# Performance work log

Hardware: AMD Instinct MI355X
Metric: run time of the kernel (lower is better)

## Reference

```python
import jax, jax.numpy as jnp
import numpy as np

GROUPS = 8
EPS = 1e-5


def setup_inputs() -> dict:
    key = jax.random.key(0)
    ks = jax.random.split(key, 7)
    B, C, H, W = 16, 512, 32, 32
    x = jax.random.normal(ks[0], (B, C, H, W), dtype=jnp.float32)
    norm_w = jnp.ones((C,), jnp.float32)
    norm_b = jnp.zeros((C,), jnp.float32)
    qkv_w = jax.random.normal(ks[1], (3 * C, C), dtype=jnp.float32) * (1.0 / np.sqrt(C))
    qkv_b = jnp.zeros((3 * C,), jnp.float32)
    proj_w = jax.random.normal(ks[2], (C, C), dtype=jnp.float32) * (1.0 / np.sqrt(C))
    proj_b = jnp.zeros((C,), jnp.float32)
    num_heads = 8
    return {"x": x, "norm_w": norm_w, "norm_b": norm_b, "qkv_w": qkv_w,
            "qkv_b": qkv_b, "proj_w": proj_w, "proj_b": proj_b,
            "num_heads": num_heads}


def reference(x, norm_w, norm_b, qkv_w, qkv_b, proj_w, proj_b, num_heads):
    b, c, h, w = x.shape
    n = h * w
    x_in = x
    # GroupNorm(8, c): normalize over (channels-in-group, spatial)
    xg = x.reshape(b, GROUPS, c // GROUPS, n)
    mean = jnp.mean(xg, axis=(2, 3), keepdims=True)
    var = jnp.var(xg, axis=(2, 3), keepdims=True)
    xn = (xg - mean) * jax.lax.rsqrt(var + EPS)
    xn = xn.reshape(b, c, n) * norm_w[None, :, None] + norm_b[None, :, None]
    # 1x1 Conv1d == per-position matmul
    qkv = jnp.einsum('oc,bcn->bon', qkv_w, xn) + qkv_b[None, :, None]
    q, k, v = jnp.split(qkv, 3, axis=1)
    d = c // num_heads
    q = q.reshape(b, num_heads, d, n)
    k = k.reshape(b, num_heads, d, n)
    v = v.reshape(b, num_heads, d, n)
    scale = 1.0 / np.sqrt(d).astype(np.float32)
    # note: scale applied to BOTH q and k (as in the torch source)
    attn = jnp.einsum('bhdn,bhdm->bhnm', q * scale, k * scale)
    attn = jax.nn.softmax(attn, axis=-1)
    out = jnp.einsum('bhnm,bhdm->bhdn', attn, v).reshape(b, c, n)
    out = jnp.einsum('oc,bcn->bon', proj_w, out) + proj_b[None, :, None]
    return out.reshape(b, c, h, w) + x_in
```

## Files before the change

### kernel.cpp

```cpp
#include <hip/hip_runtime.h>

#define NB 16
#define NC 512
#define NSP 1024
#define OQKV 1536
#define EPSV 1e-5f

typedef unsigned short u16;
typedef unsigned int u32;
typedef __attribute__((ext_vector_type(8))) short short8;
typedef __attribute__((ext_vector_type(4))) float f32x4;

__device__ __forceinline__ float us2f(u16 u) {
  return __uint_as_float(((u32)u) << 16);
}
__device__ __forceinline__ u16 f2us(float f) {
  u32 x = __float_as_uint(f);
  return (u16)((x + 0x7fffu + ((x >> 16) & 1u)) >> 16);
}
#if __has_builtin(__builtin_amdgcn_cvt_pk_bf16_f32)
typedef __attribute__((ext_vector_type(2))) __bf16 bf16x2_t;
__device__ __forceinline__ u32 pack2(float a, float b) {
  bf16x2_t r = __builtin_amdgcn_cvt_pk_bf16_f32(a, b);
  return *reinterpret_cast<u32*>(&r);
}
#else
__device__ __forceinline__ u32 pack2(float a, float b) {
  return (u32)f2us(a) | ((u32)f2us(b) << 16);
}
#endif
__device__ __forceinline__ float ld1(const void* p, size_t i, bool f32) {
  return f32 ? ((const float*)p)[i] : us2f(((const u16*)p)[i]);
}
__device__ __forceinline__ bool detect_f32(const void* x0) {
  const u32* xw = (const u32*)x0;
  u32 w = xw[threadIdx.x & 63];
  u32 e = ((w & 0xffffu) >> 7) & 0xffu;
  bool sane = (e >= 0x60u && e <= 0x9fu);
  return __popcll(__ballot(sane)) < 32;
}

typedef const __attribute__((address_space(1))) unsigned int* gas_t;
typedef __attribute__((address_space(3))) unsigned int* las_t;
__device__ __forceinline__ void gload16(const void* g, void* l) {
  __builtin_amdgcn_global_load_lds((gas_t)g, (las_t)l, 16, 0, 0);
}

__global__ __launch_bounds__(256) void gn_partial(
    const void* __restrict__ x, float2* __restrict__ part) {
  bool f32 = detect_f32(x);
  int idx = blockIdx.x;
  size_t base = (size_t)idx * 32768;
  float s1 = 0.f, s2 = 0.f;
  for (int i = threadIdx.x; i < 4096; i += 256) {
    float f[8];
    if (f32) {
      float4 a = *((const float4*)x + (base >> 2) + i * 2);
      float4 b = *((const float4*)x + (base >> 2) + i * 2 + 1);
      f[0]=a.x; f[1]=a.y; f[2]=a.z; f[3]=a.w; f[4]=b.x; f[5]=b.y; f[6]=b.z; f[7]=b.w;
    } else {
      uint4 p = *((const uint4*)x + (base >> 3) + i);
      f[0]=us2f((u16)(p.x&0xffffu)); f[1]=us2f((u16)(p.x>>16));
      f[2]=us2f((u16)(p.y&0xffffu)); f[3]=us2f((u16)(p.y>>16));
      f[4]=us2f((u16)(p.z&0xffffu)); f[5]=us2f((u16)(p.z>>16));
      f[6]=us2f((u16)(p.w&0xffffu)); f[7]=us2f((u16)(p.w>>16));
    }
#pragma unroll
    for (int m = 0; m < 8; m++) { s1 += f[m]; s2 += f[m] * f[m]; }
  }
  __shared__ float r1[256], r2[256];
  r1[threadIdx.x] = s1; r2[threadIdx.x] = s2;
  __syncthreads();
  for (int s = 128; s > 0; s >>= 1) {
    if ((int)threadIdx.x < s) {
      r1[threadIdx.x] += r1[threadIdx.x + s];
      r2[threadIdx.x] += r2[threadIdx.x + s];
    }
    __syncthreads();
  }
  if (threadIdx.x == 0) part[idx] = make_float2(r1[0], r2[0]);
}

__global__ __launch_bounds__(256) void prep_all(
    const void* __restrict__ x, const float2* __restrict__ part,
    const void* __restrict__ gamma, const void* __restrict__ beta,
    const void* __restrict__ qkvw, const void* __restrict__ projw,
    u16* __restrict__ wq, u16* __restrict__ wp, u16* __restrict__ xnt) {
  bool f32 = detect_f32(x);
  int p = blockIdx.x;
  int t = threadIdx.x;
  if (p < 512) {
    const void* src = (p < 384) ? qkvw : projw;
    u16* dst = (p < 384) ? wq : wp;
    size_t e = ((size_t)(p < 384 ? p : p - 384) * 256 + t) * 8;
    uint4 v;
    if (f32) {
      float4 a = *(const float4*)((const float*)src + e);
      float4 b = *(const float4*)((const float*)src + e + 4);
      v.x = pack2(a.x, a.y); v.y = pack2(a.z, a.w);
      v.z = pack2(b.x, b.y); v.w = pack2(b.z, b.w);
    } else {
      v = *(const uint4*)((const u16*)src + e);
    }
    *(uint4*)(dst + e) = v;
    return;
  }
  int q = p - 512;
  int b = q >> 7;
  int c0 = ((q >> 4) & 7) << 6;
  int n0 = (q & 15) << 6;
  __shared__ __align__(16) u16 T[64 * 64];
  int cc = t >> 4;
  int nn = (t & 15) << 2;
  float2 pa = part[((b << 3) + (c0 >> 6)) * 2];
  float2 pb = part[((b << 3) + (c0 >> 6)) * 2 + 1];
  float mean = (pa.x + pb.x) * (1.f / 65536.f);
  float var = (pa.y + pb.y) * (1.f / 65536.f) - mean * mean;
  float inv = rsqrtf(var + EPSV);
#pragma unroll
  for (int rep = 0; rep < 4; rep++) {
    int cl = cc + (rep << 4);
    int c = c0 + cl;
    float g = ld1(gamma, c, f32), be = ld1(beta, c, f32);
    float wsc = g * inv, bsc = be - mean * wsc;
    size_t xb = ((size_t)b * NC + c) * NSP + n0 + nn;
    float f[4];
    if (f32) {
      float4 v = *(const float4*)((const float*)x + xb);
      f[0]=v.x; f[1]=v.y; f[2]=v.z; f[3]=v.w;
    } else {
      uint2 v = *(const uint2*)((const u16*)x + xb);
      f[0]=us2f((u16)(v.x&0xffffu)); f[1]=us2f((u16)(v.x>>16));
      f[2]=us2f((u16)(v.y&0xffffu)); f[3]=us2f((u16)(v.y>>16));
    }
#pragma unroll
    for (int j = 0; j < 4; j++) {
      int n = nn + j;
      T[(n << 6) + (((cl & ~7) ^ ((n & 7) << 3)) | (cl & 7))] =
          f2us(fmaf(f[j], wsc, bsc));
    }
  }
  __syncthreads();
#pragma unroll
  for (int i = 0; i < 2; i++) {
    int slot = (i << 8) + t;
    int nl = slot >> 3;
    int cs = (slot & 7) << 3;
    uint4 v = *(const uint4*)&T[(nl << 6) + (cs ^ ((nl & 7) << 3))];
    *(uint4*)&xnt[((size_t)b * NSP + n0 + nl) * NC + c0 + cs] = v;
  }
}

template <bool OUTRAW, bool RES>
__global__ __launch_bounds__(256) void mfma_gemm(
    const u16* __restrict__ W, const u16* __restrict__ Xt,
    const void* __restrict__ xdet, const void* __restrict__ bias,
    const void* __restrict__ res, void* __restrict__ out, int O) {
  bool f32 = detect_f32(xdet);
  bool of = OUTRAW && f32;
  int gy = O >> 7;
  int bpb = gy << 3;
  int p = blockIdx.x + (blockIdx.y << 3) + blockIdx.z * bpb;
  int k = p >> 3;
  int b = ((p & 7) << 1) + (k >= bpb ? 1 : 0);
  int r = k - (k >= bpb ? bpb : 0);
  int orow = (r >> 3) << 7;
  int ncol = (r & 7) << 7;
  int t = threadIdx.x;
  int lane = t & 63, w = t >> 6;
  int wo = (w >> 1) << 6, wn = (w & 1) << 6;
  int l15 = lane & 15, quad = lane >> 4;

  __shared__ __align__(16) u16 Alds[128 * 64];
  __shared__ __align__(16) u16 Blds[128 * 64];

  f32x4 acc[4][4];
#pragma unroll
  for (int i = 0; i < 4; i++)
#pragma unroll
    for (int j = 0; j < 4; j++) acc[i][j] = (f32x4){0.f, 0.f, 0.f, 0.f};

  int srow = t >> 3;
  int seg = (t & 7) ^ (srow & 7);
  const u16* wpA = W + (size_t)(orow + srow) * NC + (seg << 3);
  const u16* xpB = Xt + ((size_t)b * NSP + ncol + srow) * NC + (seg << 3);

  for (int k0 = 0; k0 < NC; k0 += 64) {
    __syncthreads();
#pragma unroll
    for (int i = 0; i < 4; i++) {
      gload16(wpA + k0 + (size_t)i * (32 * NC), &Alds[(i << 11) + (w << 9)]);
      gload16(xpB + k0 + (size_t)i * (32 * NC), &Blds[(i << 11) + (w << 9)]);
    }
    __syncthreads();
#pragma unroll
    for (int kk = 0; kk < 2; kk++) {
      short8 af[4], bf[4];
#pragma unroll
      for (int ot = 0; ot < 4; ot++) {
        int rr = wo + ot * 16 + l15;
        af[ot] = *(const short8*)&Alds[(rr << 6) + ((((kk << 2) + quad) ^ (rr & 7)) << 3)];
      }
#pragma unroll
      for (int nt = 0; nt < 4; nt++) {
        int rr = wn + nt * 16 + l15;
        bf[nt] = *(const short8*)&Blds[(rr << 6) + ((((kk << 2) + quad) ^ (rr & 7)) << 3)];
      }
#pragma unroll
      for (int ot = 0; ot < 4; ot++)
#pragma unroll
        for (int nt = 0; nt < 4; nt++)
          acc[ot][nt] = __builtin_amdgcn_mfma_f32_16x16x32_bf16(
              af[ot], bf[nt], acc[ot][nt], 0, 0, 0);
    }
  }
#pragma unroll
  for (int ot = 0; ot < 4; ot++) {
#pragma unroll
    for (int rr = 0; rr < 4; rr++) {
      int o = orow + wo + ot * 16 + (quad << 2) + rr;
      float bs = ld1(bias, o, f32);
      size_t rowb = ((size_t)b * O + o) * NSP + ncol + wn + l15;
#pragma unroll
      for (int nt = 0; nt < 4; nt++) {
        size_t idx = rowb + nt * 16;
        float v = acc[ot][nt][rr] + bs;
        if (RES) v += ld1(res, idx, f32);
        if (of) ((float*)out)[idx] = v;
        else ((u16*)out)[idx] = f2us(v);
      }
    }
  }
}

__global__ __launch_bounds__(512, 4) void attn_kernel(
    const u16* __restrict__ qkv, u16* __restrict__ OT) {
  int d = blockIdx.x;
  int blk = ((((d & 7) << 4) | (d >> 5)) << 2) | ((d >> 3) & 3);
  int b = blk >> 5;
  int h = (blk >> 2) & 7;
  int q0 = (blk & 3) << 8;
  int t = threadIdx.x;
  int lane = t & 63, w = t >> 6;
  int l15 = lane & 15, quad = lane >> 4;

  __shared__ __align__(16) u16 Klds[64 * 72];
  __shared__ __align__(16) u16 Vlds[64 * 72];
  __shared__ __align__(16) u16 Plds[8][32 * 72];

  size_t hb = (size_t)b * OQKV + h * 64;

  short8 qf[2][2];
#pragma unroll
  for (int qt = 0; qt < 2; qt++)
#pragma unroll
    for (int ds = 0; ds < 2; ds++) {
      int q = q0 + (w << 5) + (qt << 4) + l15;
#pragma unroll
      for (int j = 0; j < 8; j++) {
        int dd = (ds << 5) + (quad << 3) + j;
        qf[qt][ds][j] = (short)f2us(us2f(qkv[(hb + dd) * NSP + q]) * 0.015625f);
      }
    }

  f32x4 oacc[2][4];
#pragma unroll
  for (int qt = 0; qt < 2; qt++)
#pragma unroll
    for (int dd = 0; dd < 4; dd++) oacc[qt][dd] = (f32x4){0.f, 0.f, 0.f, 0.f};
  float lsum[2] = {0.f, 0.f};

  bool isK = (t < 256);
  int ts = t & 255;
  int m0k = (ts & 15) << 2;
  int d0k = (ts >> 4) << 2;
  int sdv = ts >> 2;
  int sm0 = (ts & 3) << 4;
  const u16* kbase = qkv + (hb + 512) * NSP;
  const u16* vbase = qkv + (hb + 1024 + sdv) * NSP;
  u16* pmy = Plds[w];

  uint2 kr[4];
  uint4 vr0, vr1;
  auto preload = [&](int mc) {
    if (isK) {
#pragma unroll
      for (int i = 0; i < 4; i++)
        kr[i] = *(const uint2*)(kbase + (size_t)(d0k + i) * NSP + mc + m0k);
    } else {
      vr0 = *(const uint4*)(vbase + mc + sm0);
      vr1 = *(const uint4*)(vbase + mc + sm0 + 8);
    }
  };

  preload(0);
  for (int mc = 0; mc < NSP; mc += 64) {
    __syncthreads();
    if (isK) {
#pragma unroll
      for (int j = 0; j < 4; j++) {
        u32 s0 = (j & 2) ? kr[0].y : kr[0].x;
        u32 s1 = (j & 2) ? kr[1].y : kr[1].x;
        u32 s2 = (j & 2) ? kr[2].y : kr[2].x;
        u32 s3 = (j & 2) ? kr[3].y : kr[3].x;
        int sh = (j & 1) << 4;
        uint2 wv;
        wv.x = ((s0 >> sh) & 0xffffu) | (((s1 >> sh) & 0xffffu) << 16);
        wv.y = ((s2 >> sh) & 0xffffu) | (((s3 >> sh) & 0xffffu) << 16);
        *(uint2*)&Klds[(m0k + j) * 72 + d0k] = wv;
      }
    } else {
      *(uint4*)&Vlds[sdv * 72 + sm0] = vr0;
      *(uint4*)&Vlds[sdv * 72 + sm0 + 8] = vr1;
    }
    __syncthreads();
    if (mc + 64 < NSP) preload(mc + 64);
#pragma unroll
    for (int kg = 0; kg < 4; kg++) {
      short8 kf0 = *(const short8*)&Klds[((kg << 4) + l15) * 72 + (quad << 3)];
      short8 kf1 = *(const short8*)&Klds[((kg << 4) + l15) * 72 + 32 + (quad << 3)];
#pragma unroll
      for (int qt = 0; qt < 2; qt++) {
        f32x4 z = (f32x4){0.f, 0.f, 0.f, 0.f};
        z = __builtin_amdgcn_mfma_f32_16x16x32_bf16(kf0, qf[qt][0], z, 0, 0, 0);
        z = __builtin_amdgcn_mfma_f32_16x16x32_bf16(kf1, qf[qt][1], z, 0, 0, 0);
        float p0 = __expf(z[0]), p1 = __expf(z[1]);
        float p2 = __expf(z[2]), p3 = __expf(z[3]);
        lsum[qt] += (p0 + p1) + (p2 + p3);
        uint2 pw;
        pw.x = pack2(p0, p1); pw.y = pack2(p2, p3);
        *(uint2*)&pmy[((qt << 4) + l15) * 72 + (kg << 4) + (quad << 2)] = pw;
      }
    }
#pragma unroll
    for (int mg = 0; mg < 2; mg++) {
      short8 pf0 = *(const short8*)&pmy[l15 * 72 + (mg << 5) + (quad << 3)];
      short8 pf1 = *(const short8*)&pmy[(16 + l15) * 72 + (mg << 5) + (quad << 3)];
#pragma unroll
      for (int dd = 0; dd < 4; dd++) {
        short8 vf = *(const short8*)&Vlds[((dd << 4) + l15) * 72 + (mg << 5) + (quad << 3)];
        oacc[0][dd] = __builtin_amdgcn_mfma_f32_16x16x32_bf16(vf, pf0, oacc[0][dd], 0, 0, 0);
        oacc[1][dd] = __builtin_amdgcn_mfma_f32_16x16x32_bf16(vf, pf1, oacc[1][dd], 0, 0, 0);
      }
    }
  }
  float invL[2];
#pragma unroll
  for (int qt = 0; qt < 2; qt++) {
    float v = lsum[qt];
    v += __shfl_xor(v, 16);
    v += __shfl_xor(v, 32);
    invL[qt] = 1.0f / v;
  }
#pragma unroll
  for (int qt = 0; qt < 2; qt++) {
    int q = q0 + (w << 5) + (qt << 4) + l15;
    u16* op = OT + ((size_t)b * NSP + q) * NC + (h << 6);
#pragma unroll
    for (int dd = 0; dd < 4; dd++) {
      uint2 pw;
      pw.x = pack2(oacc[qt][dd][0] * invL[qt], oacc[qt][dd][1] * invL[qt]);
      pw.y = pack2(oacc[qt][dd][2] * invL[qt], oacc[qt][dd][3] * invL[qt]);
      *(uint2*)&op[(dd << 4) + (quad << 2)] = pw;
    }
  }
}

extern "C" void kernel_launch(void* const* d_in, const int* in_sizes, int n_in,
                              void* d_out, int out_size, void* d_ws, size_t ws_size,
                              hipStream_t stream) {
  const void* x      = d_in[0];
  const void* norm_w = d_in[1];
  const void* norm_b = d_in[2];
  const void* qkv_w  = d_in[3];
  const void* qkv_b  = d_in[4];
  const void* proj_w = d_in[5];
  const void* proj_b = d_in[6];

  char* ws = (char*)d_ws;
  float2* part  = (float2*)ws;
  u16* qkv = (u16*)(ws + 4096);
  u16* xnt = (u16*)(ws + 4096 + 50331648);
  u16* wq  = (u16*)(ws + 4096 + 50331648 + 16777216);
  u16* wp  = wq + OQKV * NC;

  gn_partial<<<256, 256, 0, stream>>>(x, part);
  prep_all<<<2560, 256, 0, stream>>>(x, part, norm_w, norm_b,
                                     qkv_w, proj_w, wq, wp, xnt);
  mfma_gemm<false, false><<<dim3(8, 12, NB), 256, 0, stream>>>(
      wq, xnt, x, qkv_b, nullptr, qkv, OQKV);
  attn_kernel<<<512, 512, 0, stream>>>(qkv, xnt );
  mfma_gemm<true, true><<<dim3(8, 4, NB), 256, 0, stream>>>(
      wp, xnt, x, proj_b, x, d_out, NC);
}
```

Measured before the change: 236.9 us.

## Switch attention to 32x32x16 MFMA and pass P through registers

Rewrites the attention inner loop to use 32x32x16 bf16 MFMA tiles instead of 16x16x32. The exponentiated scores are repacked into the B-operand layout with cross-half-wave shuffles rather than a per-wave LDS round trip, and the P shared buffer is removed. This is meant to cut LDS traffic and sync pressure and raise MFMA efficiency, at the cost of larger accumulators that raise register pressure and a layout mapping that is easy to get wrong.

```diff
diff --git a/kernel.cpp b/kernel.cpp
--- a/kernel.cpp
+++ b/kernel.cpp
@@ -10,6 +10,7 @@
 typedef unsigned int u32;
 typedef __attribute__((ext_vector_type(8))) short short8;
 typedef __attribute__((ext_vector_type(4))) float f32x4;
+typedef __attribute__((ext_vector_type(16))) float f32x16;
 
 __device__ __forceinline__ float us2f(u16 u) {
   return __uint_as_float(((u32)u) << 16);
@@ -238,37 +239,33 @@
   int d = blockIdx.x;
   int blk = ((((d & 7) << 4) | (d >> 5)) << 2) | ((d >> 3) & 3);
   int b = blk >> 5;
-  int h = (blk >> 2) & 7;
+  int hh = (blk >> 2) & 7;
   int q0 = (blk & 3) << 8;
   int t = threadIdx.x;
   int lane = t & 63, w = t >> 6;
-  int l15 = lane & 15, quad = lane >> 4;
+  int l31 = lane & 31, hl = lane >> 5;
 
   __shared__ __align__(16) u16 Klds[64 * 72];
   __shared__ __align__(16) u16 Vlds[64 * 72];
-  __shared__ __align__(16) u16 Plds[8][32 * 72];
-
-  size_t hb = (size_t)b * OQKV + h * 64;
-
-  short8 qf[2][2];
-#pragma unroll
-  for (int qt = 0; qt < 2; qt++)
-#pragma unroll
-    for (int ds = 0; ds < 2; ds++) {
-      int q = q0 + (w << 5) + (qt << 4) + l15;
-#pragma unroll
-      for (int j = 0; j < 8; j++) {
-        int dd = (ds << 5) + (quad << 3) + j;
-        qf[qt][ds][j] = (short)f2us(us2f(qkv[(hb + dd) * NSP + q]) * 0.015625f);
-      }
-    }
-
-  f32x4 oacc[2][4];
-#pragma unroll
-  for (int qt = 0; qt < 2; qt++)
-#pragma unroll
-    for (int dd = 0; dd < 4; dd++) oacc[qt][dd] = (f32x4){0.f, 0.f, 0.f, 0.f};
-  float lsum[2] = {0.f, 0.f};
+
+  size_t hb = (size_t)b * OQKV + hh * 64;
+  int qrow = q0 + (w << 5) + l31;
+
+  short8 qf[4];
+#pragma unroll
+  for (int ks = 0; ks < 4; ks++)
+#pragma unroll
+    for (int j = 0; j < 8; j++) {
+      int dd = ks * 16 + (hl << 3) + j;
+      qf[ks][j] = (short)f2us(us2f(qkv[(hb + dd) * NSP + qrow]) * 0.015625f);
+    }
+
+  f32x16 oacc[2];
+#pragma unroll
+  for (int dt = 0; dt < 2; dt++)
+#pragma unroll
+    for (int e = 0; e < 16; e++) oacc[dt][e] = 0.f;
+  float lsum = 0.f;
 
   bool isK = (t < 256);
   int ts = t & 255;
@@ -278,7 +275,6 @@
   int sm0 = (ts & 3) << 4;
   const u16* kbase = qkv + (hb + 512) * NSP;
   const u16* vbase = qkv + (hb + 1024 + sdv) * NSP;
-  u16* pmy = Plds[w];
 
   uint2 kr[4];
   uint4 vr0, vr1;
@@ -316,54 +312,57 @@
     __syncthreads();
     if (mc + 64 < NSP) preload(mc + 64);
 #pragma unroll
-    for (int kg = 0; kg < 4; kg++) {
-      short8 kf0 = *(const short8*)&Klds[((kg << 4) + l15) * 72 + (quad << 3)];
-      short8 kf1 = *(const short8*)&Klds[((kg << 4) + l15) * 72 + 32 + (quad << 3)];
-#pragma unroll
-      for (int qt = 0; qt < 2; qt++) {
-        f32x4 z = (f32x4){0.f, 0.f, 0.f, 0.f};
-        z = __builtin_amdgcn_mfma_f32_16x16x32_bf16(kf0, qf[qt][0], z, 0, 0, 0);
-        z = __builtin_amdgcn_mfma_f32_16x16x32_bf16(kf1, qf[qt][1], z, 0, 0, 0);
-        float p0 = __expf(z[0]), p1 = __expf(z[1]);
-        float p2 = __expf(z[2]), p3 = __expf(z[3]);
-        lsum[qt] += (p0 + p1) + (p2 + p3);
-        uint2 pw;
-        pw.x = pack2(p0, p1); pw.y = pack2(p2, p3);
-        *(uint2*)&pmy[((qt << 4) + l15) * 72 + (kg << 4) + (quad << 2)] = pw;
-      }
-    }
-#pragma unroll
-    for (int mg = 0; mg < 2; mg++) {
-      short8 pf0 = *(const short8*)&pmy[l15 * 72 + (mg << 5) + (quad << 3)];
-      short8 pf1 = *(const short8*)&pmy[(16 + l15) * 72 + (mg << 5) + (quad << 3)];
-#pragma unroll
-      for (int dd = 0; dd < 4; dd++) {
-        short8 vf = *(const short8*)&Vlds[((dd << 4) + l15) * 72 + (mg << 5) + (quad << 3)];
-        oacc[0][dd] = __builtin_amdgcn_mfma_f32_16x16x32_bf16(vf, pf0, oacc[0][dd], 0, 0, 0);
-        oacc[1][dd] = __builtin_amdgcn_mfma_f32_16x16x32_bf16(vf, pf1, oacc[1][dd], 0, 0, 0);
-      }
-    }
-  }
-  float invL[2];
-#pragma unroll
-  for (int qt = 0; qt < 2; qt++) {
-    float v = lsum[qt];
-    v += __shfl_xor(v, 16);
-    v += __shfl_xor(v, 32);
-    invL[qt] = 1.0f / v;
-  }
-#pragma unroll
-  for (int qt = 0; qt < 2; qt++) {
-    int q = q0 + (w << 5) + (qt << 4) + l15;
-    u16* op = OT + ((size_t)b * NSP + q) * NC + (h << 6);
-#pragma unroll
-    for (int dd = 0; dd < 4; dd++) {
+    for (int mt = 0; mt < 2; mt++) {
+      f32x16 s;
+#pragma unroll
+      for (int e = 0; e < 16; e++) s[e] = 0.f;
+#pragma unroll
+      for (int ks = 0; ks < 4; ks++) {
+        short8 kf = *(const short8*)&Klds[((mt << 5) + l31) * 72 + (ks << 4) + (hl << 3)];
+        s = __builtin_amdgcn_mfma_f32_32x32x16_bf16(kf, qf[ks], s, 0, 0, 0);
+      }
+      u32 pk[8];
+#pragma unroll
+      for (int i = 0; i < 8; i++) {
+        float e0 = __expf(s[2 * i]), e1 = __expf(s[2 * i + 1]);
+        lsum += e0 + e1;
+        pk[i] = pack2(e0, e1);
+      }
+      short8 pf[2];
+#pragma unroll
+      for (int ks2 = 0; ks2 < 2; ks2++) {
+        u32 o0 = pk[4 * ks2], o1 = pk[4 * ks2 + 1];
+        u32 o2 = pk[4 * ks2 + 2], o3 = pk[4 * ks2 + 3];
+        u32 r0 = (u32)__shfl_xor((int)(hl ? o0 : o2), 32);
+        u32 r1 = (u32)__shfl_xor((int)(hl ? o1 : o3), 32);
+        uint4 wv;
+        wv.x = hl ? r0 : o0;
+        wv.y = hl ? r1 : o1;
+        wv.z = hl ? o2 : r0;
+        wv.w = hl ? o3 : r1;
+        pf[ks2] = *reinterpret_cast<short8*>(&wv);
+      }
+#pragma unroll
+      for (int dt = 0; dt < 2; dt++)
+#pragma unroll
+        for (int ks2 = 0; ks2 < 2; ks2++) {
+          short8 vf = *(const short8*)&Vlds[((dt << 5) + l31) * 72 + (mt << 5) + (ks2 << 4) + (hl << 3)];
+          oacc[dt] = __builtin_amdgcn_mfma_f32_32x32x16_bf16(vf, pf[ks2], oacc[dt], 0, 0, 0);
+        }
+    }
+  }
+  float tot = lsum + __shfl_xor(lsum, 32);
+  float invL = 1.0f / tot;
+  u16* op = OT + ((size_t)b * NSP + qrow) * NC + (hh << 6);
+#pragma unroll
+  for (int dt = 0; dt < 2; dt++)
+#pragma unroll
+    for (int g = 0; g < 4; g++) {
       uint2 pw;
-      pw.x = pack2(oacc[qt][dd][0] * invL[qt], oacc[qt][dd][1] * invL[qt]);
-      pw.y = pack2(oacc[qt][dd][2] * invL[qt], oacc[qt][dd][3] * invL[qt]);
-      *(uint2*)&op[(dd << 4) + (quad << 2)] = pw;
-    }
-  }
+      pw.x = pack2(oacc[dt][4 * g + 0] * invL, oacc[dt][4 * g + 1] * invL);
+      pw.y = pack2(oacc[dt][4 * g + 2] * invL, oacc[dt][4 * g + 3] * invL);
+      *(uint2*)&op[(dt << 5) + (g << 3) + (hl << 2)] = pw;
+    }
 }
 
 extern "C" void kernel_launch(void* const* d_in, const int* in_sizes, int n_in,
```

New measurement: 232.9 us. About the same (-1.7%).
